# Kernel tuning notes

Hardware: AMD Instinct MI355X
Metric: run time of the kernel (lower is better)

Reference implementation:

```python
import jax, jax.numpy as jnp
import numpy as np

T, B, NINP, NHID = 1024, 64, 2048, 2048


def setup_inputs() -> dict:
    key = jax.random.key(0)
    ks = jax.random.split(key, 10)
    s = 0.02  # small init for numerical sanity (torch code used uniform(0,1))
    return {
        "x": jax.random.normal(ks[0], (T, B, NINP), dtype=jnp.float32),
        "hidden": jax.random.normal(ks[1], (B, NHID), dtype=jnp.float32),
        "W_cx": jax.random.normal(ks[2], (NHID, NINP), dtype=jnp.float32) * s,
        "W_ih": jax.random.normal(ks[3], (NHID, NHID), dtype=jnp.float32) * s,
        "W_ix": jax.random.normal(ks[4], (NHID, NINP), dtype=jnp.float32) * s,
        "W_fh": jax.random.normal(ks[5], (NHID, NHID), dtype=jnp.float32) * s,
        "W_fx": jax.random.normal(ks[6], (NHID, NINP), dtype=jnp.float32) * s,
        "b_i": jnp.zeros((NHID,), dtype=jnp.float32),
        "b_f": jnp.zeros((NHID,), dtype=jnp.float32),
    }


def reference(x, hidden, W_cx, W_ih, W_ix, W_fh, W_fx, b_i, b_f):
    # Precompute all input-side projections in big batched GEMMs (same math,
    # hoisted out of the sequential loop).
    content = jnp.einsum('tbi,hi->tbh', x, W_cx)            # [T,B,H]
    ix = jnp.einsum('tbi,hi->tbh', x, W_ix) + b_i            # [T,B,H]
    fx = jnp.einsum('tbi,hi->tbh', x, W_fx) + b_f            # [T,B,H]

    def step(h, inp):
        c_t, ix_t, fx_t = inp
        i_t = jax.nn.sigmoid(h @ W_ih.T + ix_t)
        f_t = jax.nn.sigmoid(h @ W_fh.T + fx_t)
        h_new = jnp.tanh(i_t * c_t + f_t * h)
        return h_new, h_new

    nexth, output = jax.lax.scan(step, hidden, (content, ix, fx))
    return output, nexth
```

## Files before the change

### kernel.cpp

```cpp
#include <hip/hip_runtime.h>
#include <cstdint>
#include <cstddef>

#define T_SEQ 1024
#define BATCH 64
#define NH 2048

typedef _Float16 half8 __attribute__((ext_vector_type(8)));
typedef _Float16 half4 __attribute__((ext_vector_type(4)));
typedef float f32x4 __attribute__((ext_vector_type(4)));
typedef unsigned u32x2 __attribute__((ext_vector_type(2)));

__device__ inline void gload_lds16(const void* g, void* l) {
    __builtin_amdgcn_global_load_lds(
        (const __attribute__((address_space(1))) uint32_t*)g,
        (__attribute__((address_space(3))) uint32_t*)l,
        16, 0, 0);
}

#define LLC_ST2(addr, val)                                                   \
    asm volatile("global_store_short %0, %1, off sc0 sc1"                    \
                 :: "v"(addr), "v"(val) : "memory")
#define LLC_ST4(addr, val)                                                   \
    asm volatile("global_store_dword %0, %1, off sc0 sc1"                    \
                 :: "v"(addr), "v"(val) : "memory")
#define LLC_ST4F(addr, val)                                                  \
    asm volatile("global_store_dword %0, %1, off sc0 sc1"                    \
                 :: "v"(addr), "v"(val) : "memory")
#define LLC_LD8(dst, addr)                                                   \
    asm volatile("global_load_dwordx2 %0, %1, off sc0 sc1\n\ts_waitcnt vmcnt(0)" \
                 : "=v"(dst) : "v"(addr))

__global__ __launch_bounds__(256) void cvt_f32_f16(const float* __restrict__ src,
                                                   _Float16* __restrict__ dst,
                                                   long long n) {
    long long i = ((long long)blockIdx.x * 256 + threadIdx.x) * 4;
    long long stride = (long long)gridDim.x * 256 * 4;
    for (; i < n; i += stride) {
        const float4 v = *(const float4*)(src + i);
        half4 o;
        o[0] = (_Float16)v.x; o[1] = (_Float16)v.y;
        o[2] = (_Float16)v.z; o[3] = (_Float16)v.w;
        *(half4*)(dst + i) = o;
    }
}

__global__ __launch_bounds__(256) void proj_gemm(const _Float16* __restrict__ A,
                                                 const _Float16* __restrict__ B,
                                                 _Float16* __restrict__ C, int M) {
    __shared__ _Float16 As[128][64];
    __shared__ _Float16 Bs[128][64];
    const int NBN = 48;
    const int nbm = M >> 7;
    const int nwg = nbm * NBN;
    const int per = nwg >> 3;
    const int bid = blockIdx.x;
    const int swz = (bid & 7) * per + (bid >> 3);
    const int bm = swz / NBN, bn = swz % NBN;

    const int tid = threadIdx.x;
    const int lane = tid & 63, w = tid >> 6;
    const int wm = w & 1, wn = w >> 1;

    f32x4 acc[4][4] = {};

    const int srow = lane >> 3;
    const int scol = (lane & 7) * 8;

    for (int bk = 0; bk < NH / 64; ++bk) {
#pragma unroll
        for (int i = 0; i < 4; ++i) {
            int r = w * 32 + i * 8;
            const _Float16* gA = A + (size_t)(bm * 128 + r + srow) * NH + bk * 64 + scol;
            gload_lds16(gA, &As[r][0]);
            const _Float16* gB = B + (size_t)(bn * 128 + r + srow) * NH + bk * 64 + scol;
            gload_lds16(gB, &Bs[r][0]);
        }
        __syncthreads();
#pragma unroll
        for (int kk = 0; kk < 2; ++kk) {
            half8 af[4], bf[4];
#pragma unroll
            for (int mi = 0; mi < 4; ++mi)
                af[mi] = *(const half8*)&As[wm * 64 + mi * 16 + (lane & 15)][kk * 32 + (lane >> 4) * 8];
#pragma unroll
            for (int ni = 0; ni < 4; ++ni)
                bf[ni] = *(const half8*)&Bs[wn * 64 + ni * 16 + (lane & 15)][kk * 32 + (lane >> 4) * 8];
#pragma unroll
            for (int mi = 0; mi < 4; ++mi)
#pragma unroll
                for (int ni = 0; ni < 4; ++ni)
                    acc[mi][ni] = __builtin_amdgcn_mfma_f32_16x16x32_f16(af[mi], bf[ni], acc[mi][ni], 0, 0, 0);
        }
        __syncthreads();
    }
#pragma unroll
    for (int mi = 0; mi < 4; ++mi)
#pragma unroll
        for (int ni = 0; ni < 4; ++ni)
#pragma unroll
            for (int r = 0; r < 4; ++r) {
                int m = bm * 128 + wm * 64 + mi * 16 + (lane >> 4) * 4 + r;
                int n = bn * 128 + wn * 64 + ni * 16 + (lane & 15);
                C[(size_t)m * 6144 + n] = (_Float16)acc[mi][ni][r];
            }
}

__global__ __launch_bounds__(512, 1) void scan_kernel(
    const _Float16* __restrict__ proj,
    const _Float16* __restrict__ Wr,
    _Float16* hb0, _Float16* hb1,
    const float* __restrict__ b_i, const float* __restrict__ b_f,
    float* __restrict__ out,
    unsigned* flags, int t0, int nsteps) {
    extern __shared__ char smem[];
    _Float16* Wlds = (_Float16*)smem;
    float* red = (float*)(smem + 131072);

    const int wg = blockIdx.x;
    const int xcd = wg & 7;
    const int slot = wg >> 3;
    const int g = slot & 1;
    const int idx = xcd * 16 + (slot >> 1);
    const int j0 = idx * 16;
    const int b0 = g * 32;
    unsigned* flags_g = flags + g * 256;

    const int tid = threadIdx.x;
    const int lane = tid & 63;
    const int w = tid >> 6;
    const int mi = w & 1;
    const int kq = w >> 1;

    for (int q = 0; q < 16; ++q) {
        int e = q * 512 + tid;
        int l = e & 63;
        int fk = (e >> 6) & 63;
        int gate = e >> 12;
        const _Float16* src = Wr + ((size_t)gate << 22) +
                              (size_t)(j0 + (l & 15)) * NH + fk * 32 + (l >> 4) * 8;
        *(half8*)(Wlds + ((size_t)(gate * 64 + fk) * 64 + l) * 8) = *(const half8*)src;
    }

    const float bi_s = b_i[j0 + (lane & 15)];
    const float bf_s = b_f[j0 + (lane & 15)];

    float hprev[4], pc[4], pix[4], pfx[4];
    if (kq == 0) {
        const _Float16* hini = (t0 & 1) ? hb1 : hb0;
#pragma unroll
        for (int r = 0; r < 4; ++r) {
            int b = b0 + mi * 16 + (lane >> 4) * 4 + r;
            int j = j0 + (lane & 15);
            unsigned tmp;
            asm volatile("global_load_ushort %0, %1, off sc0 sc1\n\ts_waitcnt vmcnt(0)"
                         : "=v"(tmp) : "v"(hini + (size_t)b * NH + j));
            hprev[r] = (float)__builtin_bit_cast(_Float16, (unsigned short)tmp);
            size_t pbase = ((size_t)b) * 6144 + j;
            pc[r] = (float)proj[pbase];
            pix[r] = (float)proj[pbase + 2048];
            pfx[r] = (float)proj[pbase + 4096];
        }
    }

    __syncthreads();

    for (int s = 0; s < nsteps; ++s) {
        const int t = t0 + s;
        const _Float16* hcur = (t & 1) ? hb1 : hb0;
        _Float16* hnxt = (t & 1) ? hb0 : hb1;

        half8 afr[16];
        const _Float16* hrow = hcur + (size_t)(b0 + mi * 16 + (lane & 15)) * NH +
                               kq * 512 + (lane >> 4) * 8;
#pragma unroll
        for (int u = 0; u < 16; ++u) afr[u] = *(const half8*)(hrow + u * 32);

        f32x4 ai0 = {}, ai1 = {}, af0 = {}, af1 = {};
#pragma unroll
        for (int u = 0; u < 16; ++u) {
            int fk = kq * 16 + u;
            half8 wi = *(const half8*)(Wlds + ((size_t)fk * 64 + lane) * 8);
            half8 wf = *(const half8*)(Wlds + ((size_t)(64 + fk) * 64 + lane) * 8);
            if (u & 1) {
                ai1 = __builtin_amdgcn_mfma_f32_16x16x32_f16(afr[u], wi, ai1, 0, 0, 0);
                af1 = __builtin_amdgcn_mfma_f32_16x16x32_f16(afr[u], wf, af1, 0, 0, 0);
            } else {
                ai0 = __builtin_amdgcn_mfma_f32_16x16x32_f16(afr[u], wi, ai0, 0, 0, 0);
                af0 = __builtin_amdgcn_mfma_f32_16x16x32_f16(afr[u], wf, af0, 0, 0, 0);
            }
        }
        f32x4 acc_i = ai0 + ai1;
        f32x4 acc_f = af0 + af1;

        if (kq != 0) {
            const int sl = mi * 3 + (kq - 1);
#pragma unroll
            for (int r = 0; r < 4; ++r) {
                red[(sl * 8 + r) * 64 + lane] = acc_i[r];
                red[(sl * 8 + 4 + r) * 64 + lane] = acc_f[r];
            }
        }
        __syncthreads();

        float hn_keep[4];
        if (kq == 0) {
#pragma unroll
            for (int p = 0; p < 3; ++p) {
                const int sl = mi * 3 + p;
#pragma unroll
                for (int r = 0; r < 4; ++r) {
                    acc_i[r] += red[(sl * 8 + r) * 64 + lane];
                    acc_f[r] += red[(sl * 8 + 4 + r) * 64 + lane];
                }
            }
#pragma unroll
            for (int r = 0; r < 4; ++r) {
                int b = b0 + mi * 16 + (lane >> 4) * 4 + r;
                int j = j0 + (lane & 15);
                float iv = 1.0f / (1.0f + __expf(-(acc_i[r] + pix[r] + bi_s)));
                float fv = 1.0f / (1.0f + __expf(-(acc_f[r] + pfx[r] + bf_s)));
                float z = iv * pc[r] + fv * hprev[r];
                float hn = 1.0f - 2.0f / (__expf(2.0f * z) + 1.0f);
                hprev[r] = hn;
                hn_keep[r] = hn;
                _Float16 hn16 = (_Float16)hn;
                LLC_ST2(hnxt + (size_t)b * NH + j, hn16);
            }
        }
        __syncthreads();

        const unsigned tv = (unsigned)(t + 1);
        if (tid == 0) {
            unsigned* myflag = flags_g + idx;
            LLC_ST4(myflag, tv);
        }
        if (kq == 0) {
#pragma unroll
            for (int r = 0; r < 4; ++r) {
                int b = b0 + mi * 16 + (lane >> 4) * 4 + r;
                int j = j0 + (lane & 15);
                float* oaddr = out + (size_t)t * (BATCH * NH) + (size_t)b * NH + j;
                LLC_ST4F(oaddr, hn_keep[r]);
                if (t == T_SEQ - 1) {
                    float* faddr = out + (size_t)T_SEQ * (BATCH * NH) + (size_t)b * NH + j;
                    LLC_ST4F(faddr, hn_keep[r]);
                }
            }
            if (s + 1 < nsteps) {
#pragma unroll
                for (int r = 0; r < 4; ++r) {
                    int b = b0 + mi * 16 + (lane >> 4) * 4 + r;
                    int j = j0 + (lane & 15);
                    size_t pbase = ((size_t)(s + 1) * 64 + b) * 6144 + j;
                    pc[r] = (float)proj[pbase];
                    pix[r] = (float)proj[pbase + 2048];
                    pfx[r] = (float)proj[pbase + 4096];
                }
            }
        }
        if (w == 0) {
            const unsigned* fb = flags_g + lane * 2;
            while (true) {
                u32x2 v;
                LLC_LD8(v, fb);
                if (__all(v[0] >= tv && v[1] >= tv)) break;
                __builtin_amdgcn_s_sleep(1);
            }
            __builtin_amdgcn_fence(__ATOMIC_ACQUIRE, "agent");
        }
        __syncthreads();
    }
}

extern "C" void kernel_launch(void* const* d_in, const int* in_sizes, int n_in,
                              void* d_out, int out_size, void* d_ws, size_t ws_size,
                              hipStream_t stream) {
    const float* x = (const float*)d_in[0];
    const float* hidden = (const float*)d_in[1];
    const float* W_cx = (const float*)d_in[2];
    const float* W_ih = (const float*)d_in[3];
    const float* W_ix = (const float*)d_in[4];
    const float* W_fh = (const float*)d_in[5];
    const float* W_fx = (const float*)d_in[6];
    const float* b_i = (const float*)d_in[7];
    const float* b_f = (const float*)d_in[8];
    float* out = (float*)d_out;

    char* ws = (char*)d_ws;
    size_t off = 0;
    auto alloc = [&](size_t bytes) {
        char* p = ws + off;
        off += (bytes + 255) & ~(size_t)255;
        return p;
    };
    _Float16* Wp = (_Float16*)alloc((size_t)6144 * NH * 2);
    _Float16* Wr = (_Float16*)alloc((size_t)2 * NH * NH * 2);
    _Float16* hb0 = (_Float16*)alloc((size_t)BATCH * NH * 2);
    _Float16* hb1 = (_Float16*)alloc((size_t)BATCH * NH * 2);
    unsigned* flags = (unsigned*)alloc(4096);
    const size_t fixed = off;

    int chunk = 32;
    for (int c = T_SEQ; c >= 32; c >>= 1) {
        size_t need = fixed + (size_t)c * 64 * NH * 2 + (size_t)c * 64 * 6144 * 2 + 1024;
        if (need <= ws_size) { chunk = c; break; }
    }
    _Float16* xh = (_Float16*)alloc((size_t)chunk * 64 * NH * 2);
    _Float16* proj = (_Float16*)alloc((size_t)chunk * 64 * 6144 * 2);

    hipMemsetAsync(flags, 0, 4096, stream);

    const long long wsz = (long long)NH * NH;
    cvt_f32_f16<<<2048, 256, 0, stream>>>(W_cx, Wp, wsz);
    cvt_f32_f16<<<2048, 256, 0, stream>>>(W_ix, Wp + wsz, wsz);
    cvt_f32_f16<<<2048, 256, 0, stream>>>(W_fx, Wp + 2 * wsz, wsz);
    cvt_f32_f16<<<2048, 256, 0, stream>>>(W_ih, Wr, wsz);
    cvt_f32_f16<<<2048, 256, 0, stream>>>(W_fh, Wr + wsz, wsz);
    cvt_f32_f16<<<128, 256, 0, stream>>>(hidden, hb0, (long long)BATCH * NH);

    const int nch = T_SEQ / chunk;
    for (int c = 0; c < nch; ++c) {
        const int t0 = c * chunk;
        const int M = chunk * 64;
        cvt_f32_f16<<<2048, 256, 0, stream>>>(x + (size_t)t0 * 64 * NH, xh, (long long)M * NH);
        proj_gemm<<<dim3((M / 128) * 48), 256, 0, stream>>>(xh, Wp, proj, M);
        scan_kernel<<<256, 512, 143360, stream>>>(proj, Wr, hb0, hb1, b_i, b_f,
                                                  out, flags, t0, chunk);
    }
}
```

Baseline: 10.62 ms.

## Split recurrent GEMM across workgroups by K with partial-sum exchange and finer flags

Changes the scan kernel's decomposition so each workgroup owns 64 hidden columns and one quarter of the K dimension instead of 16 columns over full K. Each workgroup then only needs a 512-wide slice of h per step, which it stages into swizzled LDS. Partial sums from three K-slices are exchanged through global memory with per-column-group flags, and a finer per-slice h-ready flag replaces the global all-workgroup barrier. This aims to cut per-step h traffic and barrier width. In exchange it adds an extra cross-workgroup handoff (partial store, flag, poll, load) on the critical path of each step.

Result: faster. 9.895 ms (-6.8%).

```diff
diff --git a/kernel.cpp b/kernel.cpp
--- a/kernel.cpp
+++ b/kernel.cpp
@@ -9,7 +9,7 @@
 typedef _Float16 half8 __attribute__((ext_vector_type(8)));
 typedef _Float16 half4 __attribute__((ext_vector_type(4)));
 typedef float f32x4 __attribute__((ext_vector_type(4)));
-typedef unsigned u32x2 __attribute__((ext_vector_type(2)));
+typedef unsigned u32x4 __attribute__((ext_vector_type(4)));
 
 __device__ inline void gload_lds16(const void* g, void* l) {
     __builtin_amdgcn_global_load_lds(
@@ -18,18 +18,28 @@
         16, 0, 0);
 }
 
+#define LLC_LD16NW(dst, addr)                                                \
+    asm volatile("global_load_dwordx4 %0, %1, off sc0 sc1"                   \
+                 : "=v"(dst) : "v"(addr))
+#define LLC_LD4(dst, addr)                                                   \
+    asm volatile("global_load_dword %0, %1, off sc0 sc1\n\ts_waitcnt vmcnt(0)" \
+                 : "=v"(dst) : "v"(addr))
+#define LLC_LD16W(dst, addr)                                                 \
+    asm volatile("global_load_dwordx4 %0, %1, off sc0 sc1\n\ts_waitcnt vmcnt(0)" \
+                 : "=v"(dst) : "v"(addr))
 #define LLC_ST2(addr, val)                                                   \
     asm volatile("global_store_short %0, %1, off sc0 sc1"                    \
                  :: "v"(addr), "v"(val) : "memory")
 #define LLC_ST4(addr, val)                                                   \
     asm volatile("global_store_dword %0, %1, off sc0 sc1"                    \
                  :: "v"(addr), "v"(val) : "memory")
-#define LLC_ST4F(addr, val)                                                  \
-    asm volatile("global_store_dword %0, %1, off sc0 sc1"                    \
+#define LLC_ST16(addr, val)                                                  \
+    asm volatile("global_store_dwordx4 %0, %1, off sc0 sc1"                  \
                  :: "v"(addr), "v"(val) : "memory")
-#define LLC_LD8(dst, addr)                                                   \
-    asm volatile("global_load_dwordx2 %0, %1, off sc0 sc1\n\ts_waitcnt vmcnt(0)" \
-                 : "=v"(dst) : "v"(addr))
+
+__device__ inline void wait_vm0() {
+    asm volatile("s_waitcnt vmcnt(0)" ::: "memory");
+}
 
 __global__ __launch_bounds__(256) void cvt_f32_f16(const float* __restrict__ src,
                                                    _Float16* __restrict__ dst,
@@ -112,51 +122,59 @@
     _Float16* hb0, _Float16* hb1,
     const float* __restrict__ b_i, const float* __restrict__ b_f,
     float* __restrict__ out,
-    unsigned* flags, int t0, int nsteps) {
+    unsigned* hflags, unsigned* pflags, float* part,
+    int t0, int nsteps) {
     extern __shared__ char smem[];
     _Float16* Wlds = (_Float16*)smem;
-    float* red = (float*)(smem + 131072);
+    char* hstage = smem + 131072;
 
     const int wg = blockIdx.x;
     const int xcd = wg & 7;
     const int slot = wg >> 3;
     const int g = slot & 1;
-    const int idx = xcd * 16 + (slot >> 1);
-    const int j0 = idx * 16;
+    const int rem = slot >> 1;
+    const int js = xcd * 4 + (rem & 3);
+    const int ks = rem >> 2;
+    const int j0g = js * 64;
     const int b0 = g * 32;
-    unsigned* flags_g = flags + g * 256;
+    const int k0 = ks * 512;
 
     const int tid = threadIdx.x;
     const int lane = tid & 63;
     const int w = tid >> 6;
     const int mi = w & 1;
-    const int kq = w >> 1;
+    const int nt = w >> 1;
+
+    unsigned* hflags_g = hflags + g * 32;
+    unsigned* pflags_g = pflags + g * 128;
 
     for (int q = 0; q < 16; ++q) {
         int e = q * 512 + tid;
-        int l = e & 63;
-        int fk = (e >> 6) & 63;
+        int le = e & 63;
+        int u = (e >> 6) & 15;
+        int nte = (e >> 10) & 3;
         int gate = e >> 12;
         const _Float16* src = Wr + ((size_t)gate << 22) +
-                              (size_t)(j0 + (l & 15)) * NH + fk * 32 + (l >> 4) * 8;
-        *(half8*)(Wlds + ((size_t)(gate * 64 + fk) * 64 + l) * 8) = *(const half8*)src;
-    }
-
-    const float bi_s = b_i[j0 + (lane & 15)];
-    const float bf_s = b_f[j0 + (lane & 15)];
+            (size_t)(j0g + nte * 16 + (le & 15)) * NH + k0 + u * 32 + (le >> 4) * 8;
+        *(half8*)(Wlds + (((size_t)(gate * 4 + nte) * 16 + u) * 64 + le) * 8) =
+            *(const half8*)src;
+    }
+
+    const int jj = j0g + nt * 16 + (lane & 15);
+    const float bi_s = b_i[jj];
+    const float bf_s = b_f[jj];
 
     float hprev[4], pc[4], pix[4], pfx[4];
-    if (kq == 0) {
+    if (ks == 0) {
         const _Float16* hini = (t0 & 1) ? hb1 : hb0;
 #pragma unroll
         for (int r = 0; r < 4; ++r) {
             int b = b0 + mi * 16 + (lane >> 4) * 4 + r;
-            int j = j0 + (lane & 15);
             unsigned tmp;
             asm volatile("global_load_ushort %0, %1, off sc0 sc1\n\ts_waitcnt vmcnt(0)"
-                         : "=v"(tmp) : "v"(hini + (size_t)b * NH + j));
+                         : "=v"(tmp) : "v"(hini + (size_t)b * NH + jj));
             hprev[r] = (float)__builtin_bit_cast(_Float16, (unsigned short)tmp);
-            size_t pbase = ((size_t)b) * 6144 + j;
+            size_t pbase = (size_t)b * 6144 + jj;
             pc[r] = (float)proj[pbase];
             pix[r] = (float)proj[pbase + 2048];
             pfx[r] = (float)proj[pbase + 4096];
@@ -169,107 +187,125 @@
         const int t = t0 + s;
         const _Float16* hcur = (t & 1) ? hb1 : hb0;
         _Float16* hnxt = (t & 1) ? hb0 : hb1;
-
-        half8 afr[16];
-        const _Float16* hrow = hcur + (size_t)(b0 + mi * 16 + (lane & 15)) * NH +
-                               kq * 512 + (lane >> 4) * 8;
-#pragma unroll
-        for (int u = 0; u < 16; ++u) afr[u] = *(const half8*)(hrow + u * 32);
-
-        f32x4 ai0 = {}, ai1 = {}, af0 = {}, af1 = {};
-#pragma unroll
-        for (int u = 0; u < 16; ++u) {
-            int fk = kq * 16 + u;
-            half8 wi = *(const half8*)(Wlds + ((size_t)fk * 64 + lane) * 8);
-            half8 wf = *(const half8*)(Wlds + ((size_t)(64 + fk) * 64 + lane) * 8);
-            if (u & 1) {
-                ai1 = __builtin_amdgcn_mfma_f32_16x16x32_f16(afr[u], wi, ai1, 0, 0, 0);
-                af1 = __builtin_amdgcn_mfma_f32_16x16x32_f16(afr[u], wf, af1, 0, 0, 0);
-            } else {
-                ai0 = __builtin_amdgcn_mfma_f32_16x16x32_f16(afr[u], wi, ai0, 0, 0, 0);
-                af0 = __builtin_amdgcn_mfma_f32_16x16x32_f16(afr[u], wf, af0, 0, 0, 0);
-            }
-        }
-        f32x4 acc_i = ai0 + ai1;
-        f32x4 acc_f = af0 + af1;
-
-        if (kq != 0) {
-            const int sl = mi * 3 + (kq - 1);
-#pragma unroll
-            for (int r = 0; r < 4; ++r) {
-                red[(sl * 8 + r) * 64 + lane] = acc_i[r];
-                red[(sl * 8 + 4 + r) * 64 + lane] = acc_f[r];
+        const unsigned tv = (unsigned)t;
+
+        if (w == 0) {
+            const unsigned* fa = hflags_g + ks * 8 + (lane & 7);
+            while (true) {
+                unsigned v;
+                LLC_LD4(v, fa);
+                if (__all((int)(v >= tv))) break;
+                __builtin_amdgcn_s_sleep(1);
             }
         }
         __syncthreads();
 
-        float hn_keep[4];
-        if (kq == 0) {
-#pragma unroll
-            for (int p = 0; p < 3; ++p) {
-                const int sl = mi * 3 + p;
-#pragma unroll
-                for (int r = 0; r < 4; ++r) {
-                    acc_i[r] += red[(sl * 8 + r) * 64 + lane];
-                    acc_f[r] += red[(sl * 8 + 4 + r) * 64 + lane];
+        {
+            half8 t0v, t1v, t2v, t3v;
+            const _Float16* srcb = hcur + (size_t)(b0 + w * 4) * NH + k0 + lane * 8;
+            LLC_LD16NW(t0v, srcb);
+            LLC_LD16NW(t1v, srcb + NH);
+            LLC_LD16NW(t2v, srcb + 2 * NH);
+            LLC_LD16NW(t3v, srcb + 3 * NH);
+            wait_vm0();
+            __builtin_amdgcn_sched_barrier(0);
+            const int r0 = w * 4;
+            *(half8*)(hstage + (r0 + 0) * 1024 + ((lane * 16) ^ (((r0 + 0) & 7) << 4))) = t0v;
+            *(half8*)(hstage + (r0 + 1) * 1024 + ((lane * 16) ^ (((r0 + 1) & 7) << 4))) = t1v;
+            *(half8*)(hstage + (r0 + 2) * 1024 + ((lane * 16) ^ (((r0 + 2) & 7) << 4))) = t2v;
+            *(half8*)(hstage + (r0 + 3) * 1024 + ((lane * 16) ^ (((r0 + 3) & 7) << 4))) = t3v;
+        }
+        __syncthreads();
+
+        f32x4 ci = {}, cf = {};
+        {
+            const int arow = mi * 16 + (lane & 15);
+            const char* abase = hstage + arow * 1024;
+            const int axor = (arow & 7) << 4;
+            const _Float16* wbi = Wlds + (((size_t)(0 * 4 + nt) * 16) * 64 + lane) * 8;
+            const _Float16* wbf = Wlds + (((size_t)(1 * 4 + nt) * 16) * 64 + lane) * 8;
+#pragma unroll
+            for (int u = 0; u < 16; ++u) {
+                half8 a = *(const half8*)(abase + ((u * 64 + (lane >> 4) * 16) ^ axor));
+                half8 wi = *(const half8*)(wbi + (size_t)u * 512);
+                half8 wf = *(const half8*)(wbf + (size_t)u * 512);
+                ci = __builtin_amdgcn_mfma_f32_16x16x32_f16(a, wi, ci, 0, 0, 0);
+                cf = __builtin_amdgcn_mfma_f32_16x16x32_f16(a, wf, cf, 0, 0, 0);
+            }
+        }
+
+        if (ks != 0) {
+            const int slotp = (((t & 1) * 2 + g) * 32 + js) * 3 + (ks - 1);
+            float* pb = part + (size_t)slotp * 4096 + w * 512 + lane * 4;
+            LLC_ST16(pb, ci);
+            LLC_ST16(pb + 256, cf);
+            wait_vm0();
+            __syncthreads();
+            if (tid == 0) LLC_ST4(pflags_g + js * 4 + (ks - 1), (unsigned)(t + 1));
+        } else {
+            if (w == 0) {
+                const unsigned* pf = pflags_g + js * 4;
+                while (true) {
+                    u32x4 v;
+                    LLC_LD16W(v, pf);
+                    if (__all((int)(v[0] >= tv + 1 && v[1] >= tv + 1 && v[2] >= tv + 1)))
+                        break;
+                    __builtin_amdgcn_s_sleep(1);
                 }
             }
+            __syncthreads();
+
+            f32x4 pi0, pg0, pi1, pg1, pi2, pg2;
+            const int sbase = (((t & 1) * 2 + g) * 32 + js) * 3;
+            const float* pb0 = part + (size_t)(sbase + 0) * 4096 + w * 512 + lane * 4;
+            const float* pb1 = part + (size_t)(sbase + 1) * 4096 + w * 512 + lane * 4;
+            const float* pb2 = part + (size_t)(sbase + 2) * 4096 + w * 512 + lane * 4;
+            LLC_LD16NW(pi0, pb0);
+            LLC_LD16NW(pg0, pb0 + 256);
+            LLC_LD16NW(pi1, pb1);
+            LLC_LD16NW(pg1, pb1 + 256);
+            LLC_LD16NW(pi2, pb2);
+            LLC_LD16NW(pg2, pb2 + 256);
+            wait_vm0();
+            __builtin_amdgcn_sched_barrier(0);
+            ci += pi0 + pi1 + pi2;
+            cf += pg0 + pg1 + pg2;
+
+            float hn_keep[4];
 #pragma unroll
             for (int r = 0; r < 4; ++r) {
                 int b = b0 + mi * 16 + (lane >> 4) * 4 + r;
-                int j = j0 + (lane & 15);
-                float iv = 1.0f / (1.0f + __expf(-(acc_i[r] + pix[r] + bi_s)));
-                float fv = 1.0f / (1.0f + __expf(-(acc_f[r] + pfx[r] + bf_s)));
+                float iv = 1.0f / (1.0f + __expf(-(ci[r] + pix[r] + bi_s)));
+                float fv = 1.0f / (1.0f + __expf(-(cf[r] + pfx[r] + bf_s)));
                 float z = iv * pc[r] + fv * hprev[r];
                 float hn = 1.0f - 2.0f / (__expf(2.0f * z) + 1.0f);
                 hprev[r] = hn;
                 hn_keep[r] = hn;
                 _Float16 hn16 = (_Float16)hn;
-                LLC_ST2(hnxt + (size_t)b * NH + j, hn16);
-            }
-        }
-        __syncthreads();
-
-        const unsigned tv = (unsigned)(t + 1);
-        if (tid == 0) {
-            unsigned* myflag = flags_g + idx;
-            LLC_ST4(myflag, tv);
-        }
-        if (kq == 0) {
+                LLC_ST2(hnxt + (size_t)b * NH + jj, hn16);
+            }
+            wait_vm0();
+            __syncthreads();
+            if (tid == 0) LLC_ST4(hflags_g + js, (unsigned)(t + 1));
+
 #pragma unroll
             for (int r = 0; r < 4; ++r) {
                 int b = b0 + mi * 16 + (lane >> 4) * 4 + r;
-                int j = j0 + (lane & 15);
-                float* oaddr = out + (size_t)t * (BATCH * NH) + (size_t)b * NH + j;
-                LLC_ST4F(oaddr, hn_keep[r]);
-                if (t == T_SEQ - 1) {
-                    float* faddr = out + (size_t)T_SEQ * (BATCH * NH) + (size_t)b * NH + j;
-                    LLC_ST4F(faddr, hn_keep[r]);
-                }
+                out[(size_t)t * (BATCH * NH) + (size_t)b * NH + jj] = hn_keep[r];
+                if (t == T_SEQ - 1)
+                    out[(size_t)T_SEQ * (BATCH * NH) + (size_t)b * NH + jj] = hn_keep[r];
             }
             if (s + 1 < nsteps) {
 #pragma unroll
                 for (int r = 0; r < 4; ++r) {
                     int b = b0 + mi * 16 + (lane >> 4) * 4 + r;
-                    int j = j0 + (lane & 15);
-                    size_t pbase = ((size_t)(s + 1) * 64 + b) * 6144 + j;
+                    size_t pbase = ((size_t)(s + 1) * 64 + b) * 6144 + jj;
                     pc[r] = (float)proj[pbase];
                     pix[r] = (float)proj[pbase + 2048];
                     pfx[r] = (float)proj[pbase + 4096];
                 }
             }
         }
-        if (w == 0) {
-            const unsigned* fb = flags_g + lane * 2;
-            while (true) {
-                u32x2 v;
-                LLC_LD8(v, fb);
-                if (__all(v[0] >= tv && v[1] >= tv)) break;
-                __builtin_amdgcn_s_sleep(1);
-            }
-            __builtin_amdgcn_fence(__ATOMIC_ACQUIRE, "agent");
-        }
-        __syncthreads();
     }
 }
 
@@ -298,7 +334,9 @@
     _Float16* Wr = (_Float16*)alloc((size_t)2 * NH * NH * 2);
     _Float16* hb0 = (_Float16*)alloc((size_t)BATCH * NH * 2);
     _Float16* hb1 = (_Float16*)alloc((size_t)BATCH * NH * 2);
-    unsigned* flags = (unsigned*)alloc(4096);
+    unsigned* hflags = (unsigned*)alloc(256);
+    unsigned* pflags = (unsigned*)alloc(1024);
+    float* part = (float*)alloc((size_t)2 * 2 * 32 * 3 * 4096 * 4);
     const size_t fixed = off;
 
     int chunk = 32;
@@ -309,7 +347,8 @@
     _Float16* xh = (_Float16*)alloc((size_t)chunk * 64 * NH * 2);
     _Float16* proj = (_Float16*)alloc((size_t)chunk * 64 * 6144 * 2);
 
-    hipMemsetAsync(flags, 0, 4096, stream);
+    hipMemsetAsync(hflags, 0, 256, stream);
+    hipMemsetAsync(pflags, 0, 1024, stream);
 
     const long long wsz = (long long)NH * NH;
     cvt_f32_f16<<<2048, 256, 0, stream>>>(W_cx, Wp, wsz);
@@ -325,7 +364,7 @@
         const int M = chunk * 64;
         cvt_f32_f16<<<2048, 256, 0, stream>>>(x + (size_t)t0 * 64 * NH, xh, (long long)M * NH);
         proj_gemm<<<dim3((M / 128) * 48), 256, 0, stream>>>(xh, Wp, proj, M);
-        scan_kernel<<<256, 512, 143360, stream>>>(proj, Wr, hb0, hb1, b_i, b_f,
-                                                  out, flags, t0, chunk);
-    }
-}
+        scan_kernel<<<256, 512, 163840, stream>>>(proj, Wr, hb0, hb1, b_i, b_f,
+                                                  out, hflags, pflags, part, t0, chunk);
+    }
+}
```
